# Kernel optimization log

Hardware: AMD Instinct MI355X
Metric: run time of the kernel (lower is better)

The kernel has to match this reference:

```python
import jax, jax.numpy as jnp
import numpy as np

EMBED_DIM = 1024
NUM_HEADS = 16
HEAD_DIM = EMBED_DIM // NUM_HEADS
NUM_GLOBAL = 2
NUM_RANDOM = 3
WINDOW_SIZE = 3
B, S = 2, 2048


def setup_inputs() -> dict:
    key = jax.random.key(0)
    ks = jax.random.split(key, 10)
    scale = 0.02
    inp = {
        "x": jax.random.normal(ks[0], (B, S, EMBED_DIM), dtype=jnp.float32),
        "random_indices": jax.random.randint(ks[1], (S, NUM_RANDOM), 0, S, dtype=jnp.int32),
        "q_w": jax.random.normal(ks[2], (EMBED_DIM, EMBED_DIM), dtype=jnp.float32) * scale,
        "q_b": jnp.zeros((EMBED_DIM,), dtype=jnp.float32),
        "k_w": jax.random.normal(ks[3], (EMBED_DIM, EMBED_DIM), dtype=jnp.float32) * scale,
        "k_b": jnp.zeros((EMBED_DIM,), dtype=jnp.float32),
        "v_w": jax.random.normal(ks[4], (EMBED_DIM, EMBED_DIM), dtype=jnp.float32) * scale,
        "v_b": jnp.zeros((EMBED_DIM,), dtype=jnp.float32),
        "o_w": jax.random.normal(ks[5], (EMBED_DIM, EMBED_DIM), dtype=jnp.float32) * scale,
        "o_b": jnp.zeros((EMBED_DIM,), dtype=jnp.float32),
    }
    return inp


def _build_mask(random_indices, seq_len):
    # [S, S] boolean BigBird mask: global rows/cols + sliding window + random.
    i = jnp.arange(seq_len)[:, None]
    j = jnp.arange(seq_len)[None, :]
    glob = (i < NUM_GLOBAL) | (j < NUM_GLOBAL)
    win = jnp.abs(i - j) <= WINDOW_SIZE
    rand = jnp.zeros((seq_len, seq_len), dtype=bool)
    rows = jnp.repeat(jnp.arange(seq_len), NUM_RANDOM)
    rand = rand.at[rows, random_indices.reshape(-1)].set(True)
    return glob | win | rand


def reference(x, random_indices, q_w, q_b, k_w, k_b, v_w, v_b, o_w, o_b):
    b, s, _ = x.shape
    # torch nn.Linear: y = x @ W.T + b
    q = (x @ q_w.T + q_b).reshape(b, s, NUM_HEADS, HEAD_DIM).transpose(0, 2, 1, 3)
    k = (x @ k_w.T + k_b).reshape(b, s, NUM_HEADS, HEAD_DIM).transpose(0, 2, 1, 3)
    v = (x @ v_w.T + v_b).reshape(b, s, NUM_HEADS, HEAD_DIM).transpose(0, 2, 1, 3)
    scores = jnp.einsum("bhqd,bhkd->bhqk", q, k) / jnp.sqrt(jnp.float32(HEAD_DIM))
    mask = _build_mask(random_indices, s)  # [S, S]
    scores = jnp.where(mask[None, None, :, :], scores, -jnp.inf)
    probs = jax.nn.softmax(scores, axis=-1)
    out = jnp.einsum("bhqk,bhkd->bhqd", probs, v)
    out = out.transpose(0, 2, 1, 3).reshape(b, s, EMBED_DIM)
    return out @ o_w.T + o_b
```

## Files before the change

### kernel.cpp

```cpp
#include <hip/hip_runtime.h>

#define B_  2
#define S_  2048
#define E_  1024
#define H_  16
#define D_  64
#define NGLOB 2
#define NRAND 3
#define WIN 3

typedef __bf16 bf16x8 __attribute__((ext_vector_type(8)));
typedef float  f32x4  __attribute__((ext_vector_type(4)));

__device__ __forceinline__ unsigned short f2bf(float f) {
    unsigned u = __builtin_bit_cast(unsigned, f);
    unsigned r = u + 0x7FFFu + ((u >> 16) & 1u);
    return (unsigned short)(r >> 16);
}
__device__ __forceinline__ float bf2f(unsigned short u) {
    return __builtin_bit_cast(float, (unsigned)u << 16);
}

__device__ __forceinline__ void g2l16(const unsigned short* g, unsigned short* l) {
    __builtin_amdgcn_global_load_lds(
        (const __attribute__((address_space(1))) unsigned*)g,
        (__attribute__((address_space(3))) unsigned*)l, 16, 0, 0);
}

__global__ __launch_bounds__(256)
void convert_all(const float* __restrict__ x,  const float* __restrict__ qw,
                 const float* __restrict__ kw, const float* __restrict__ vw,
                 const float* __restrict__ ow,
                 unsigned short* __restrict__ xb, unsigned short* __restrict__ wqkv,
                 unsigned short* __restrict__ wo) {
    const int XN = (B_ * S_ * E_) / 4;
    const int WN = (E_ * E_) / 4;
    int i = blockIdx.x * blockDim.x + threadIdx.x;
    int r, loc;
    if (i < XN) { r = 0; loc = i; }
    else        { int j = i - XN; r = 1 + (j >> 18); loc = j & (WN - 1); }
    const float* src = r == 0 ? x : r == 1 ? qw : r == 2 ? kw : r == 3 ? vw : ow;
    float4 f = ((const float4*)src)[loc];
    ushort4 u;
    u.x = f2bf(f.x); u.y = f2bf(f.y); u.z = f2bf(f.z); u.w = f2bf(f.w);
    ushort4* dst = r == 0 ? (ushort4*)xb : r == 4 ? (ushort4*)wo
                 : (ushort4*)wqkv + (size_t)(r - 1) * WN;
    dst[loc] = u;
}

__global__ __launch_bounds__(256, 3)
void gemm_qkv(const unsigned short* __restrict__ A,
              const unsigned short* __restrict__ W,
              const float* __restrict__ b0, const float* __restrict__ b1,
              const float* __restrict__ b2,
              unsigned short* __restrict__ Cb, int M, int N, int K) {
    __shared__ unsigned short sA[128 * 64];
    __shared__ unsigned short sB[128 * 64];
    const int nwg = gridDim.x;
    const int id  = (blockIdx.x & 7) * (nwg >> 3) + (blockIdx.x >> 3);
    const int bm = (id & 31) * 128;
    const int bn = (id >> 5) * 128;
    const int t = threadIdx.x;
    const int lane = t & 63;
    const int wave = t >> 6;
    const int wm = wave >> 1, wn = wave & 1;
    const int lq = lane >> 4;
    const int lr = lane & 15;

    f32x4 acc[4][4] = {};

    for (int k0 = 0; k0 < K; k0 += 64) {
        const unsigned short* Abase = A + (size_t)bm * K + k0;
        const unsigned short* Wbase = W + (size_t)bn * K + k0;
        #pragma unroll
        for (int j = 0; j < 4; ++j) {
            int c = j * 256 + t;
            int row = c >> 3, cc = c & 7;
            int gcol = ((cc ^ (row & 7)) << 3);
            int dst = j * 2048 + wave * 512;
            g2l16(Abase + (size_t)row * K + gcol, sA + dst);
            g2l16(Wbase + (size_t)row * K + gcol, sB + dst);
        }
        __syncthreads();

        #pragma unroll
        for (int ks = 0; ks < 2; ++ks) {
            const int sw = (((ks << 2) + lq) ^ (lr & 7)) << 3;
            bf16x8 af[4], bfr[4];
            #pragma unroll
            for (int i = 0; i < 4; ++i)
                af[i] = *(const bf16x8*)&sA[(wm * 64 + i * 16 + lr) * 64 + sw];
            #pragma unroll
            for (int j = 0; j < 4; ++j)
                bfr[j] = *(const bf16x8*)&sB[(wn * 64 + j * 16 + lr) * 64 + sw];
            #pragma unroll
            for (int i = 0; i < 4; ++i)
                #pragma unroll
                for (int j = 0; j < 4; ++j)
                    acc[i][j] = __builtin_amdgcn_mfma_f32_16x16x32_bf16(af[i], bfr[j], acc[i][j], 0, 0, 0);
        }
        __syncthreads();
    }

    #pragma unroll
    for (int i = 0; i < 4; ++i) {
        int row0 = bm + wm * 64 + i * 16 + lq * 4;
        #pragma unroll
        for (int j = 0; j < 4; ++j) {
            int col = bn + wn * 64 + j * 16 + lr;
            const float* bp = col < E_ ? b0 : (col < 2 * E_ ? b1 : b2);
            float bv = bp[col & (E_ - 1)];
            #pragma unroll
            for (int r = 0; r < 4; ++r)
                Cb[(size_t)(row0 + r) * N + col] = f2bf(acc[i][j][r] + bv);
        }
    }
}

__global__ __launch_bounds__(256, 3)
void gemm_o(const unsigned short* __restrict__ A,
            const unsigned short* __restrict__ W,
            const float* __restrict__ bias,
            float* __restrict__ Cf, int M, int N, int K) {
    __shared__ unsigned short sA[128 * 64];
    __shared__ unsigned short sB[128 * 64];
    const int nwg = gridDim.x;
    const int id  = (blockIdx.x & 7) * (nwg >> 3) + (blockIdx.x >> 3);
    const int bm = (id & 31) * 128;
    const int bn = (id >> 5) * 128;
    const int t = threadIdx.x;
    const int lane = t & 63;
    const int wave = t >> 6;
    const int wm = wave >> 1, wn = wave & 1;
    const int lq = lane >> 4;
    const int lr = lane & 15;

    f32x4 acc[4][4] = {};

    for (int k0 = 0; k0 < K; k0 += 64) {
        const unsigned short* Abase = A + (size_t)bm * K + k0;
        const unsigned short* Wbase = W + (size_t)bn * K + k0;
        #pragma unroll
        for (int j = 0; j < 4; ++j) {
            int c = j * 256 + t;
            int row = c >> 3, cc = c & 7;
            int gcol = ((cc ^ (row & 7)) << 3);
            int dst = j * 2048 + wave * 512;
            g2l16(Abase + (size_t)row * K + gcol, sA + dst);
            g2l16(Wbase + (size_t)row * K + gcol, sB + dst);
        }
        __syncthreads();

        #pragma unroll
        for (int ks = 0; ks < 2; ++ks) {
            const int sw = (((ks << 2) + lq) ^ (lr & 7)) << 3;
            bf16x8 af[4], bfr[4];
            #pragma unroll
            for (int i = 0; i < 4; ++i)
                af[i] = *(const bf16x8*)&sA[(wm * 64 + i * 16 + lr) * 64 + sw];
            #pragma unroll
            for (int j = 0; j < 4; ++j)
                bfr[j] = *(const bf16x8*)&sB[(wn * 64 + j * 16 + lr) * 64 + sw];
            #pragma unroll
            for (int i = 0; i < 4; ++i)
                #pragma unroll
                for (int j = 0; j < 4; ++j)
                    acc[i][j] = __builtin_amdgcn_mfma_f32_16x16x32_bf16(af[i], bfr[j], acc[i][j], 0, 0, 0);
        }
        __syncthreads();
    }

    #pragma unroll
    for (int i = 0; i < 4; ++i) {
        int row0 = bm + wm * 64 + i * 16 + lq * 4;
        #pragma unroll
        for (int j = 0; j < 4; ++j) {
            int col = bn + wn * 64 + j * 16 + lr;
            float bv = bias[col];
            #pragma unroll
            for (int r = 0; r < 4; ++r)
                Cf[(size_t)(row0 + r) * N + col] = acc[i][j][r] + bv;
        }
    }
}

__global__ __launch_bounds__(256)
void attn_fused(const unsigned short* __restrict__ qkv,
                const int* __restrict__ rnd,
                float* __restrict__ gaccp, float* __restrict__ gms,
                unsigned short* __restrict__ attn) {
    const int NB = B_ * (S_ - 2);
    int t = threadIdx.x;

    if (blockIdx.x < 512) {
        int tup = blockIdx.x >> 3, seg = blockIdx.x & 7;
        int b = tup >> 5, i = (tup >> 4) & 1, h = tup & 15;
        int w = t >> 6, l = t & 63;
        __shared__ float ps[256];
        __shared__ float red[4];
        __shared__ float ov[4][D_];

        const bf16x8* qp = (const bf16x8*)(qkv + (size_t)(b * S_ + i) * 3072 + h * D_);
        bf16x8 qv = qp[l & 7];
        float qreg[8];
        #pragma unroll
        for (int j = 0; j < 8; ++j) qreg[j] = (float)qv[j];

        const int key0 = seg * 256 + w * 64;
        float sc[8];
        #pragma unroll
        for (int it = 0; it < 8; ++it) {
            int key = key0 + it * 8 + (l >> 3);
            const bf16x8* kp = (const bf16x8*)(qkv + (size_t)(b * S_ + key) * 3072 + E_ + h * D_);
            bf16x8 kv = kp[l & 7];
            float s = 0.f;
            #pragma unroll
            for (int j = 0; j < 8; ++j) s += qreg[j] * (float)kv[j];
            s += __shfl_xor(s, 1);
            s += __shfl_xor(s, 2);
            s += __shfl_xor(s, 4);
            sc[it] = s * 0.125f;
        }
        #pragma unroll
        for (int it = 0; it < 8; ++it)
            if ((l & 7) == 0) ps[w * 64 + it * 8 + (l >> 3)] = sc[it];
        __syncthreads();

        float v = ps[t];
        float m = v;
        #pragma unroll
        for (int o = 32; o; o >>= 1) m = fmaxf(m, __shfl_xor(m, o));
        if (l == 0) red[w] = m;
        __syncthreads();
        m = fmaxf(fmaxf(red[0], red[1]), fmaxf(red[2], red[3]));
        float e = __expf(v - m);
        float sum = e;
        #pragma unroll
        for (int o = 32; o; o >>= 1) sum += __shfl_xor(sum, o);
        __syncthreads();
        if (l == 0) red[w] = sum;
        ps[t] = e;
        __syncthreads();
        if (t == 0) {
            float stot = red[0] + red[1] + red[2] + red[3];
            gms[(tup * 8 + seg) * 2]     = m;
            gms[(tup * 8 + seg) * 2 + 1] = stot;
        }

        const unsigned short* vbase =
            qkv + (size_t)(b * S_ + key0) * 3072 + 2 * E_ + h * D_ + l;
        const float* pw = ps + w * 64;
        float acc = 0.f;
        #pragma unroll 8
        for (int k = 0; k < 64; ++k)
            acc += pw[k] * bf2f(vbase[(size_t)k * 3072]);
        ov[w][l] = acc;
        __syncthreads();
        if (w == 0)
            gaccp[((size_t)tup * 8 + seg) * D_ + l] =
                ov[0][l] + ov[1][l] + ov[2][l] + ov[3][l];
        return;
    }

    int bb = blockIdx.x - 512;
    int bidx = (bb & 7) * 128 + (bb >> 3);
    int w = t >> 6, l = t & 63;
    int row = bidx * 4 + w;
    bool valid = row < NB;
    int b = row / (S_ - 2);
    int i = row % (S_ - 2) + 2;
    if (!valid) { b = 0; i = 2; }

    __shared__ int   cols_s[4][12];
    __shared__ int   ncol_sh[4];
    __shared__ float pr_s[4][16 * 13 + 3];

    const bf16x8* qp = (const bf16x8*)(qkv + (size_t)(b * S_ + i) * 3072);
    bf16x8 q0 = qp[l * 2], q1 = qp[l * 2 + 1];
    float qreg[16];
    #pragma unroll
    for (int j = 0; j < 8; ++j) { qreg[j] = (float)q0[j]; qreg[8 + j] = (float)q1[j]; }

    if (l == 0) {
        int* cols = cols_s[w];
        int n = 0;
        cols[n++] = 0; cols[n++] = 1;
        int lo = i - WIN; if (lo < NGLOB) lo = NGLOB;
        int hi = i + WIN; if (hi > S_ - 1) hi = S_ - 1;
        for (int j = lo; j <= hi; ++j) cols[n++] = j;
        for (int r = 0; r < NRAND; ++r) {
            int c = rnd[i * NRAND + r];
            bool dup = false;
            for (int q = 0; q < n; ++q) dup = dup || (cols[q] == c);
            if (!dup) cols[n++] = c;
        }
        ncol_sh[w] = n;
        for (int q = n; q < 12; ++q) cols[q] = 0;
    }
    __syncthreads();
    const int n = ncol_sh[w];
    const int h4 = l >> 2;

    float sco[12];
    #pragma unroll
    for (int c = 0; c < 12; ++c) {
        const bf16x8* kp = (const bf16x8*)(qkv + (size_t)(b * S_ + cols_s[w][c]) * 3072 + E_);
        bf16x8 k0 = kp[l * 2], k1 = kp[l * 2 + 1];
        float s = 0.f;
        #pragma unroll
        for (int j = 0; j < 8; ++j) s += qreg[j] * (float)k0[j] + qreg[8 + j] * (float)k1[j];
        s += __shfl_xor(s, 1);
        s += __shfl_xor(s, 2);
        sco[c] = (c < n) ? s * 0.125f : -1e30f;
    }

    if ((l & 3) == 0) {
        float m = -1e30f;
        #pragma unroll
        for (int c = 0; c < 12; ++c) m = fmaxf(m, sco[c]);
        float sum = 0.f;
        #pragma unroll
        for (int c = 0; c < 12; ++c) { float e = __expf(sco[c] - m); sco[c] = e; sum += e; }
        float inv = 1.f / sum;
        #pragma unroll
        for (int c = 0; c < 12; ++c) pr_s[w][h4 * 13 + c] = sco[c] * inv;
    }
    __syncthreads();

    float o[16] = {};
    #pragma unroll
    for (int c = 0; c < 12; ++c) {
        float p = pr_s[w][h4 * 13 + c];
        const bf16x8* vp = (const bf16x8*)(qkv + (size_t)(b * S_ + cols_s[w][c]) * 3072 + 2 * E_);
        bf16x8 v0 = vp[l * 2], v1 = vp[l * 2 + 1];
        #pragma unroll
        for (int j = 0; j < 8; ++j) { o[j] += p * (float)v0[j]; o[8 + j] += p * (float)v1[j]; }
    }

    if (valid) {
        ushort4 u0, u1, u2, u3;
        u0.x = f2bf(o[0]);  u0.y = f2bf(o[1]);  u0.z = f2bf(o[2]);  u0.w = f2bf(o[3]);
        u1.x = f2bf(o[4]);  u1.y = f2bf(o[5]);  u1.z = f2bf(o[6]);  u1.w = f2bf(o[7]);
        u2.x = f2bf(o[8]);  u2.y = f2bf(o[9]);  u2.z = f2bf(o[10]); u2.w = f2bf(o[11]);
        u3.x = f2bf(o[12]); u3.y = f2bf(o[13]); u3.z = f2bf(o[14]); u3.w = f2bf(o[15]);
        ushort4* op = (ushort4*)(attn + (size_t)(b * S_ + i) * E_ + l * 16);
        op[0] = u0; op[1] = u1; op[2] = u2; op[3] = u3;
    }
}

__global__ __launch_bounds__(256)
void gattn_fin(const float* __restrict__ gaccp, const float* __restrict__ gms,
               unsigned short* __restrict__ attn) {
    int gid = blockIdx.x * 256 + threadIdx.x;
    int tup = gid >> 6, d = gid & 63;
    int b = tup >> 5, i = (tup >> 4) & 1, h = tup & 15;
    float mc[8], sc[8], M = -1e30f;
    #pragma unroll
    for (int c = 0; c < 8; ++c) {
        mc[c] = gms[(tup * 8 + c) * 2];
        sc[c] = gms[(tup * 8 + c) * 2 + 1];
        M = fmaxf(M, mc[c]);
    }
    float den = 0.f, num = 0.f;
    #pragma unroll
    for (int c = 0; c < 8; ++c) {
        float f = __expf(mc[c] - M);
        den += sc[c] * f;
        num += gaccp[((size_t)tup * 8 + c) * D_ + d] * f;
    }
    attn[(size_t)(b * S_ + i) * E_ + h * D_ + d] = f2bf(num / den);
}

extern "C" void kernel_launch(void* const* d_in, const int* in_sizes, int n_in,
                              void* d_out, int out_size, void* d_ws, size_t ws_size,
                              hipStream_t stream) {
    const float* x   = (const float*)d_in[0];
    const int*   rnd = (const int*)d_in[1];
    const float* qw  = (const float*)d_in[2];
    const float* qb  = (const float*)d_in[3];
    const float* kw  = (const float*)d_in[4];
    const float* kb  = (const float*)d_in[5];
    const float* vw  = (const float*)d_in[6];
    const float* vb  = (const float*)d_in[7];
    const float* ow  = (const float*)d_in[8];
    const float* ob  = (const float*)d_in[9];
    float* out = (float*)d_out;

    char* ws = (char*)d_ws;
    unsigned short* xb    = (unsigned short*)(ws);
    unsigned short* wqkv  = (unsigned short*)(ws + 8388608);
    unsigned short* wo    = (unsigned short*)(ws + 14680064);
    unsigned short* qkv   = (unsigned short*)(ws + 16777216);
    unsigned short* attn  = (unsigned short*)(ws + 41943040);
    float*          gaccp = (float*)(ws);
    float*          gms   = (float*)(ws + 131072);

    const int M = B_ * S_;

    {
        int total4 = (M * E_ + 4 * E_ * E_) / 4;
        convert_all<<<total4 / 256, 256, 0, stream>>>(x, qw, kw, vw, ow, xb, wqkv, wo);
    }

    gemm_qkv<<<768, 256, 0, stream>>>(xb, wqkv, qb, kb, vb, qkv, M, 3 * E_, E_);

    attn_fused<<<512 + 1024, 256, 0, stream>>>(qkv, rnd, gaccp, gms, attn);

    gattn_fin<<<16, 256, 0, stream>>>(gaccp, gms, attn);

    gemm_o<<<256, 256, 0, stream>>>(attn, wo, ob, out, M, E_, E_);
}
```

Measured before the change: 169.7 us.

## Restructure global-row attention to share K/V loads across heads and both global queries

The global-query attention path is reorganized. Each block now handles one batch and a 16-key chunk for all 16 heads and both global rows, instead of one (batch, row, head) tuple over a 256-key segment. K and V rows are loaded once and reused for both global queries, and the key chunk is reduced inside the block, replacing the strided per-key V reads. The cost is a larger partial-result buffer (128 chunks per tuple) and a heavier final combine kernel that loops over 128 partials per output element.

```diff
diff --git a/kernel.cpp b/kernel.cpp
--- a/kernel.cpp
+++ b/kernel.cpp
@@ -192,77 +192,100 @@
     const int NB = B_ * (S_ - 2);
     int t = threadIdx.x;
 
-    if (blockIdx.x < 512) {
-        int tup = blockIdx.x >> 3, seg = blockIdx.x & 7;
-        int b = tup >> 5, i = (tup >> 4) & 1, h = tup & 15;
+    if (blockIdx.x < 256) {
+        int g = blockIdx.x;
+        int b = g >> 7, ck = g & 127;
         int w = t >> 6, l = t & 63;
-        __shared__ float ps[256];
-        __shared__ float red[4];
-        __shared__ float ov[4][D_];
-
-        const bf16x8* qp = (const bf16x8*)(qkv + (size_t)(b * S_ + i) * 3072 + h * D_);
-        bf16x8 qv = qp[l & 7];
-        float qreg[8];
-        #pragma unroll
-        for (int j = 0; j < 8; ++j) qreg[j] = (float)qv[j];
-
-        const int key0 = seg * 256 + w * 64;
-        float sc[8];
-        #pragma unroll
-        for (int it = 0; it < 8; ++it) {
-            int key = key0 + it * 8 + (l >> 3);
-            const bf16x8* kp = (const bf16x8*)(qkv + (size_t)(b * S_ + key) * 3072 + E_ + h * D_);
-            bf16x8 kv = kp[l & 7];
-            float s = 0.f;
-            #pragma unroll
-            for (int j = 0; j < 8; ++j) s += qreg[j] * (float)kv[j];
-            s += __shfl_xor(s, 1);
-            s += __shfl_xor(s, 2);
-            s += __shfl_xor(s, 4);
-            sc[it] = s * 0.125f;
-        }
-        #pragma unroll
-        for (int it = 0; it < 8; ++it)
-            if ((l & 7) == 0) ps[w * 64 + it * 8 + (l >> 3)] = sc[it];
+        int h = l >> 2, dseg = l & 3;
+        int key0 = ck * 16 + w * 4;
+
+        __shared__ float sm[4][16][4];
+        __shared__ float ovv[4][2][16][68];
+
+        const unsigned short* qb0 = qkv + (size_t)(b * S_) * 3072 + h * 64 + dseg * 16;
+        const unsigned short* qb1 = qb0 + 3072;
+        bf16x8 q0a = *(const bf16x8*)qb0, q0b = *(const bf16x8*)(qb0 + 8);
+        bf16x8 q1a = *(const bf16x8*)qb1, q1b = *(const bf16x8*)(qb1 + 8);
+
+        bf16x8 ka[4], kb[4], va[4], vb[4];
+        #pragma unroll
+        for (int j = 0; j < 4; ++j) {
+            const unsigned short* kr =
+                qkv + (size_t)(b * S_ + key0 + j) * 3072 + E_ + h * 64 + dseg * 16;
+            ka[j] = *(const bf16x8*)kr;  kb[j] = *(const bf16x8*)(kr + 8);
+            const unsigned short* vr = kr + E_;
+            va[j] = *(const bf16x8*)vr;  vb[j] = *(const bf16x8*)(vr + 8);
+        }
+
+        float s0[4], s1[4];
+        #pragma unroll
+        for (int j = 0; j < 4; ++j) {
+            float a0 = 0.f, a1 = 0.f;
+            #pragma unroll
+            for (int e = 0; e < 8; ++e) {
+                float k1 = (float)ka[j][e], k2 = (float)kb[j][e];
+                a0 += (float)q0a[e] * k1 + (float)q0b[e] * k2;
+                a1 += (float)q1a[e] * k1 + (float)q1b[e] * k2;
+            }
+            a0 += __shfl_xor(a0, 1); a0 += __shfl_xor(a0, 2);
+            a1 += __shfl_xor(a1, 1); a1 += __shfl_xor(a1, 2);
+            s0[j] = a0 * 0.125f; s1[j] = a1 * 0.125f;
+        }
+
+        float m0 = fmaxf(fmaxf(s0[0], s0[1]), fmaxf(s0[2], s0[3]));
+        float m1 = fmaxf(fmaxf(s1[0], s1[1]), fmaxf(s1[2], s1[3]));
+        float e0[4], e1[4], sum0 = 0.f, sum1 = 0.f;
+        #pragma unroll
+        for (int j = 0; j < 4; ++j) {
+            e0[j] = __expf(s0[j] - m0); sum0 += e0[j];
+            e1[j] = __expf(s1[j] - m1); sum1 += e1[j];
+        }
+        float o0[16] = {}, o1[16] = {};
+        #pragma unroll
+        for (int j = 0; j < 4; ++j)
+            #pragma unroll
+            for (int e = 0; e < 8; ++e) {
+                float v1 = (float)va[j][e], v2 = (float)vb[j][e];
+                o0[e] += e0[j] * v1;  o0[8 + e] += e0[j] * v2;
+                o1[e] += e1[j] * v1;  o1[8 + e] += e1[j] * v2;
+            }
+
+        if (dseg == 0) {
+            sm[w][h][0] = m0; sm[w][h][1] = sum0;
+            sm[w][h][2] = m1; sm[w][h][3] = sum1;
+        }
+        #pragma unroll
+        for (int e = 0; e < 16; ++e) {
+            ovv[w][0][h][dseg * 16 + e] = o0[e];
+            ovv[w][1][h][dseg * 16 + e] = o1[e];
+        }
         __syncthreads();
 
-        float v = ps[t];
-        float m = v;
-        #pragma unroll
-        for (int o = 32; o; o >>= 1) m = fmaxf(m, __shfl_xor(m, o));
-        if (l == 0) red[w] = m;
-        __syncthreads();
-        m = fmaxf(fmaxf(red[0], red[1]), fmaxf(red[2], red[3]));
-        float e = __expf(v - m);
-        float sum = e;
-        #pragma unroll
-        for (int o = 32; o; o >>= 1) sum += __shfl_xor(sum, o);
-        __syncthreads();
-        if (l == 0) red[w] = sum;
-        ps[t] = e;
-        __syncthreads();
-        if (t == 0) {
-            float stot = red[0] + red[1] + red[2] + red[3];
-            gms[(tup * 8 + seg) * 2]     = m;
-            gms[(tup * 8 + seg) * 2 + 1] = stot;
-        }
-
-        const unsigned short* vbase =
-            qkv + (size_t)(b * S_ + key0) * 3072 + 2 * E_ + h * D_ + l;
-        const float* pw = ps + w * 64;
-        float acc = 0.f;
-        #pragma unroll 8
-        for (int k = 0; k < 64; ++k)
-            acc += pw[k] * bf2f(vbase[(size_t)k * 3072]);
-        ov[w][l] = acc;
-        __syncthreads();
-        if (w == 0)
-            gaccp[((size_t)tup * 8 + seg) * D_ + l] =
-                ov[0][l] + ov[1][l] + ov[2][l] + ov[3][l];
+        #pragma unroll
+        for (int r = 0; r < 8; ++r) {
+            int ot = r * 256 + t;
+            int ii = ot >> 10, hh = (ot >> 6) & 15, d = ot & 63;
+            float M = -1e30f;
+            #pragma unroll
+            for (int ww = 0; ww < 4; ++ww) M = fmaxf(M, sm[ww][hh][ii * 2]);
+            float den = 0.f, num = 0.f;
+            #pragma unroll
+            for (int ww = 0; ww < 4; ++ww) {
+                float f = __expf(sm[ww][hh][ii * 2] - M);
+                den += sm[ww][hh][ii * 2 + 1] * f;
+                num += ovv[ww][ii][hh][d] * f;
+            }
+            int tup = b * 32 + ii * 16 + hh;
+            gaccp[((size_t)tup * 128 + ck) * D_ + d] = num;
+            if (d == 0) {
+                gms[((size_t)tup * 128 + ck) * 2]     = M;
+                gms[((size_t)tup * 128 + ck) * 2 + 1] = den;
+            }
+        }
         return;
     }
 
-    int bb = blockIdx.x - 512;
+    int bb = blockIdx.x - 256;
     int bidx = (bb & 7) * 128 + (bb >> 3);
     int w = t >> 6, l = t & 63;
     int row = bidx * 4 + w;
@@ -354,19 +377,15 @@
     int gid = blockIdx.x * 256 + threadIdx.x;
     int tup = gid >> 6, d = gid & 63;
     int b = tup >> 5, i = (tup >> 4) & 1, h = tup & 15;
-    float mc[8], sc[8], M = -1e30f;
-    #pragma unroll
-    for (int c = 0; c < 8; ++c) {
-        mc[c] = gms[(tup * 8 + c) * 2];
-        sc[c] = gms[(tup * 8 + c) * 2 + 1];
-        M = fmaxf(M, mc[c]);
-    }
+    float M = -1e30f;
+    #pragma unroll 8
+    for (int c = 0; c < 128; ++c) M = fmaxf(M, gms[((size_t)tup * 128 + c) * 2]);
     float den = 0.f, num = 0.f;
-    #pragma unroll
-    for (int c = 0; c < 8; ++c) {
-        float f = __expf(mc[c] - M);
-        den += sc[c] * f;
-        num += gaccp[((size_t)tup * 8 + c) * D_ + d] * f;
+    #pragma unroll 8
+    for (int c = 0; c < 128; ++c) {
+        float f = __expf(gms[((size_t)tup * 128 + c) * 2] - M);
+        den += gms[((size_t)tup * 128 + c) * 2 + 1] * f;
+        num += gaccp[((size_t)tup * 128 + c) * D_ + d] * f;
     }
     attn[(size_t)(b * S_ + i) * E_ + h * D_ + d] = f2bf(num / den);
 }
@@ -393,7 +412,7 @@
     unsigned short* qkv   = (unsigned short*)(ws + 16777216);
     unsigned short* attn  = (unsigned short*)(ws + 41943040);
     float*          gaccp = (float*)(ws);
-    float*          gms   = (float*)(ws + 131072);
+    float*          gms   = (float*)(ws + 2097152);
 
     const int M = B_ * S_;
 
@@ -404,7 +423,7 @@
 
     gemm_qkv<<<768, 256, 0, stream>>>(xb, wqkv, qb, kb, vb, qkv, M, 3 * E_, E_);
 
-    attn_fused<<<512 + 1024, 256, 0, stream>>>(qkv, rnd, gaccp, gms, attn);
+    attn_fused<<<256 + 1024, 256, 0, stream>>>(qkv, rnd, gaccp, gms, attn);
 
     gattn_fin<<<16, 256, 0, stream>>>(gaccp, gms, attn);
 
```

Result: slower. 184.1 us (+8.5%).
